# Kernel tuning notes

Hardware: AMD Instinct MI355X
Metric: run time of the kernel (lower is better)

Reference implementation:

```python
import jax, jax.numpy as jnp
import numpy as np

EPS = 1e-5
QMAX = 127.0


def fake_quant_int8(x):
    """Per-tensor symmetric int8 fake-quant (quantize+dequantize), dynamic scale.
    Mirrors brevitas Int8ActPerTensorFloat / Int8WeightPerTensorFloat math."""
    scale = jnp.maximum(jnp.max(jnp.abs(x)) / QMAX, 1e-8)
    q = jnp.clip(jnp.round(x / scale), -128.0, 127.0) * scale
    # straight-through estimator (identity grad through quant)
    return x + jax.lax.stop_gradient(q - x)


def layer_norm(x, g, b):
    mu = jnp.mean(x, axis=-1, keepdims=True)
    var = jnp.mean(jnp.square(x - mu), axis=-1, keepdims=True)
    return (x - mu) * jax.lax.rsqrt(var + EPS) * g + b


def setup_inputs() -> dict:
    key = jax.random.key(0)
    B, S, D, H = 64, 196, 768, 12
    M = 4 * D
    ks = jax.random.split(key, 8)
    s = lambda d: 1.0 / np.sqrt(d)
    return {
        "x": jax.random.normal(ks[0], (B, S, D), jnp.float32),
        "ln1_g": jnp.ones((D,), jnp.float32),
        "ln1_b": jnp.zeros((D,), jnp.float32),
        "ln2_g": jnp.ones((D,), jnp.float32),
        "ln2_b": jnp.zeros((D,), jnp.float32),
        "w_qkv": jax.random.normal(ks[1], (D, 3 * D), jnp.float32) * s(D),
        "b_qkv": jnp.zeros((3 * D,), jnp.float32),
        "w_o": jax.random.normal(ks[2], (D, D), jnp.float32) * s(D),
        "b_o": jnp.zeros((D,), jnp.float32),
        "w1": jax.random.normal(ks[3], (D, M), jnp.float32) * s(D),
        "b1": jnp.zeros((M,), jnp.float32),
        "w2": jax.random.normal(ks[4], (M, D), jnp.float32) * s(M),
        "b2": jnp.zeros((D,), jnp.float32),
    }


def _block(x, ln1_g, ln1_b, ln2_g, ln2_b, w_qkv, b_qkv, w_o, b_o, w1, b1, w2, b2):
    B, S, D = x.shape
    H = 12
    hd = D // H

    # --- LN -> quant -> MHSA -> add ---
    r1 = x
    h = fake_quant_int8(layer_norm(x, ln1_g, ln1_b))
    qkv = jnp.einsum("bsd,de->bse", h, fake_quant_int8(w_qkv)) + b_qkv
    q, k, v = jnp.split(qkv, 3, axis=-1)
    q = q.reshape(B, S, H, hd)
    k = k.reshape(B, S, H, hd)
    v = v.reshape(B, S, H, hd)
    logits = jnp.einsum("bqhd,bkhd->bhqk", q, k) / jnp.sqrt(jnp.float32(hd))
    attn = jax.nn.softmax(logits, axis=-1)
    ctx = jnp.einsum("bhqk,bkhd->bqhd", attn, v).reshape(B, S, D)
    ctx = fake_quant_int8(ctx)
    mhsa = jnp.einsum("bsd,de->bse", ctx, fake_quant_int8(w_o)) + b_o
    x = mhsa + r1

    # --- LN -> quant -> MLP (fc1 -> GELU -> quant -> fc2) -> add ---
    r2 = x
    h = fake_quant_int8(layer_norm(x, ln2_g, ln2_b))
    h = jnp.einsum("bsd,dm->bsm", h, fake_quant_int8(w1)) + b1
    h = jax.nn.gelu(h, approximate=False)  # torch nn.GELU default = exact erf
    h = fake_quant_int8(h)
    h = jnp.einsum("bsm,md->bsd", h, fake_quant_int8(w2)) + b2
    return h + r2


def reference(x, ln1_g, ln1_b, ln2_g, ln2_b, w_qkv, b_qkv, w_o, b_o, w1, b1, w2, b2):
    return _block(x, ln1_g, ln1_b, ln2_g, ln2_b, w_qkv, b_qkv, w_o, b_o, w1, b1, w2, b2)
```

## Files before the change

kernel.cpp:

```cpp
#include <hip/hip_runtime.h>
#include <cstdint>
#include <cstddef>

#define DEVFN __device__ __forceinline__

typedef short bf16x8 __attribute__((ext_vector_type(8)));
typedef float f32x4  __attribute__((ext_vector_type(4)));
typedef int   i32x4  __attribute__((ext_vector_type(4)));

static constexpr int NTOK  = 64 * 196;
static constexpr int DMODEL= 768;
static constexpr int NHEAD = 12;
static constexpr int NQKV  = 2304;
static constexpr int MMLP  = 3072;
static constexpr int SEQ   = 196;
static constexpr int NBATCH= 64;

enum { SL_LN1=0, SL_WQKV=1, SL_CTX=2, SL_WO=3, SL_LN2=4, SL_W1=5, SL_GELU=6, SL_W2=7 };

static constexpr int NSH       = 64;
static constexpr int SH_STRIDE = 64;
static constexpr int SLOTS_U32 = NSH * SH_STRIDE;

DEVFN float bf2f(unsigned short u){ return __uint_as_float(((unsigned)u) << 16); }
DEVFN unsigned short f2bf(float f){
  unsigned u = __float_as_uint(f);
  u += 0x7fffu + ((u >> 16) & 1u);
  return (unsigned short)(u >> 16);
}
DEVFN void split_bf(float v, unsigned short& hi, unsigned short& lo){
  hi = f2bf(v);
  lo = f2bf(v - bf2f(hi));
}
DEVFN float slot_absmax(const unsigned* __restrict__ slots, int slot){
  unsigned m = 0u;
#pragma unroll
  for (int j = 0; j < NSH; j++){
    unsigned u = slots[j * SH_STRIDE + slot];
    m = (u > m) ? u : m;
  }
  return __uint_as_float(m);
}
DEVFN float slot_scale(const unsigned* __restrict__ slots, int slot){
  return fmaxf(slot_absmax(slots, slot) / 127.0f, 1e-8f);
}
DEVFN void scatter_amax(unsigned* slots, int slot, unsigned bucket, float v){
  atomicMax(slots + (bucket & (NSH - 1)) * SH_STRIDE + slot, __float_as_uint(v));
}
DEVFN float quantval(float x, float s){
  float q = rintf(x / s);
  return fminf(fmaxf(q, -128.0f), 127.0f);
}
DEVFN unsigned pack4(float a, float b, float c, float d){
  return  ((unsigned)(unsigned char)(char)(int)a)
        | ((unsigned)(unsigned char)(char)(int)b << 8)
        | ((unsigned)(unsigned char)(char)(int)c << 16)
        | ((unsigned)(unsigned char)(char)(int)d << 24);
}
DEVFN float gelu_fast(float v){
  float s  = v * 0.70710678118654752f;
  float ax = fabsf(s);
  float t  = __builtin_amdgcn_rcpf(fmaf(0.3275911f, ax, 1.0f));
  float p  = t * fmaf(t, fmaf(t, fmaf(t, fmaf(t, 1.061405429f, -1.453152027f),
                                      1.421413741f), -0.284496736f), 0.254829592f);
  float er = fmaf(-p, __expf(-ax * ax), 1.0f);
  unsigned sgn = __float_as_uint(s) & 0x80000000u;
  er = __uint_as_float(__float_as_uint(er) | sgn);
  return 0.5f * v * (1.0f + er);
}
DEVFN f32x4 mfma16(bf16x8 a, bf16x8 b, f32x4 c){
  return __builtin_amdgcn_mfma_f32_16x16x32_bf16(a, b, c, 0, 0, 0);
}
DEVFN i32x4 mfma16i8(i32x4 a, i32x4 b, i32x4 c){
  return __builtin_amdgcn_mfma_i32_16x16x64_i8(a, b, c, 0, 0, 0);
}
DEVFN void async_ld16(const void* g, void* lds){
  __builtin_amdgcn_global_load_lds((const __attribute__((address_space(1))) void*)g,
                                   (__attribute__((address_space(3))) void*)lds, 16, 0, 0);
}
DEVFN int vidx(int d, int s){
  return d * 256 + (s ^ (((d ^ (d >> 2)) & 7) << 3));
}

__global__ void k_init(unsigned* slots){
  int i = blockIdx.x * blockDim.x + threadIdx.x;
  if (i < SLOTS_U32) slots[i] = 0u;
}

__global__ void k_absmax4(const float* __restrict__ x0, const float* __restrict__ x1,
                          const float* __restrict__ x2, const float* __restrict__ x3,
                          unsigned* slots){
  int bid = blockIdx.x;
  const float* x; int n4, slot, b0, nb;
  if (bid < 256)      { x = x0; n4 = DMODEL * NQKV  / 4; slot = SL_WQKV; b0 = 0;   nb = 256; }
  else if (bid < 384) { x = x1; n4 = DMODEL * DMODEL/ 4; slot = SL_WO;   b0 = 256; nb = 128; }
  else if (bid < 640) { x = x2; n4 = DMODEL * MMLP  / 4; slot = SL_W1;   b0 = 384; nb = 256; }
  else                { x = x3; n4 = MMLP   * DMODEL/ 4; slot = SL_W2;   b0 = 640; nb = 256; }
  int lb = bid - b0;
  float m = 0.f;
  const float4* x4 = (const float4*)x;
  int stride = nb * blockDim.x;
  for (int j = lb * blockDim.x + threadIdx.x; j < n4; j += stride){
    float4 v = x4[j];
    m = fmaxf(m, fmaxf(fmaxf(fabsf(v.x), fabsf(v.y)), fmaxf(fabsf(v.z), fabsf(v.w))));
  }
  for (int off = 32; off; off >>= 1) m = fmaxf(m, __shfl_xor(m, off));
  __shared__ float wm[4];
  int lane = threadIdx.x & 63, w = threadIdx.x >> 6;
  if (lane == 0) wm[w] = m;
  __syncthreads();
  if (threadIdx.x == 0){
    float bm = fmaxf(fmaxf(wm[0], wm[1]), fmaxf(wm[2], wm[3]));
    scatter_amax(slots, slot, bid, bm);
  }
}

__global__ void k_quant_transpose(const float* __restrict__ w, char* __restrict__ wt,
                                  int K, int N, const unsigned* __restrict__ slots, int slot){
  __shared__ float tile[32][33];
  float s = slot_scale(slots, slot);
  int n0 = blockIdx.x * 32, k0 = blockIdx.y * 32;
  int tx = threadIdx.x & 31, ty = threadIdx.x >> 5;
#pragma unroll
  for (int i = 0; i < 4; i++){
    int k = k0 + ty + i * 8;
    float v = w[(size_t)k * N + n0 + tx];
    tile[ty + i * 8][tx] = quantval(v, s);
  }
  __syncthreads();
  int n = threadIdx.x >> 3, kg = threadIdx.x & 7;
  unsigned o = pack4(tile[kg * 4 + 0][n], tile[kg * 4 + 1][n],
                     tile[kg * 4 + 2][n], tile[kg * 4 + 3][n]);
  *(unsigned*)(wt + (size_t)(n0 + n) * K + k0 + kg * 4) = o;
}

__global__ void k_layernorm(const float* __restrict__ x, const float* __restrict__ g,
                            const float* __restrict__ b, float* __restrict__ out,
                            unsigned* slots, int slot){
  int w = threadIdx.x >> 6, lane = threadIdx.x & 63;
  int row = blockIdx.x * 4 + w;
  const float4* xr = (const float4*)(x + (size_t)row * DMODEL);
  float4 v[3];
  float sum = 0.f;
#pragma unroll
  for (int i = 0; i < 3; i++){ v[i] = xr[i * 64 + lane]; sum += v[i].x + v[i].y + v[i].z + v[i].w; }
  for (int off = 32; off; off >>= 1) sum += __shfl_xor(sum, off);
  float mu = sum * (1.0f / 768.0f);
  float vs = 0.f;
#pragma unroll
  for (int i = 0; i < 3; i++){
    float dx = v[i].x - mu, dy = v[i].y - mu, dz = v[i].z - mu, dw = v[i].w - mu;
    vs += dx * dx + dy * dy + dz * dz + dw * dw;
  }
  for (int off = 32; off; off >>= 1) vs += __shfl_xor(vs, off);
  float inv = 1.0f / sqrtf(vs * (1.0f / 768.0f) + 1e-5f);
  const float4* g4 = (const float4*)g; const float4* b4 = (const float4*)b;
  float4* o4 = (float4*)(out + (size_t)row * DMODEL);
  float am = 0.f;
#pragma unroll
  for (int i = 0; i < 3; i++){
    float4 gg = g4[i * 64 + lane], bb = b4[i * 64 + lane], o;
    o.x = (v[i].x - mu) * inv * gg.x + bb.x;
    o.y = (v[i].y - mu) * inv * gg.y + bb.y;
    o.z = (v[i].z - mu) * inv * gg.z + bb.z;
    o.w = (v[i].w - mu) * inv * gg.w + bb.w;
    am = fmaxf(am, fmaxf(fmaxf(fabsf(o.x), fabsf(o.y)), fmaxf(fabsf(o.z), fabsf(o.w))));
    o4[i * 64 + lane] = o;
  }
  for (int off = 32; off; off >>= 1) am = fmaxf(am, __shfl_xor(am, off));
  __shared__ float am4[4];
  if (lane == 0) am4[w] = am;
  __syncthreads();
  if (threadIdx.x == 0){
    float bm = fmaxf(fmaxf(am4[0], am4[1]), fmaxf(am4[2], am4[3]));
    scatter_amax(slots, slot, blockIdx.x, bm);
  }
}

__global__ void k_quant_act(const float* __restrict__ x, unsigned* __restrict__ out,
                            int n4, const unsigned* __restrict__ slots, int slot){
  float s = slot_scale(slots, slot);
  const float4* x4 = (const float4*)x;
  int stride = gridDim.x * blockDim.x;
  for (int j = blockIdx.x * blockDim.x + threadIdx.x; j < n4; j += stride){
    float4 v = x4[j];
    out[j] = pack4(quantval(v.x, s), quantval(v.y, s), quantval(v.z, s), quantval(v.w, s));
  }
}

__global__ void k_quant_bf16_i8(const unsigned short* __restrict__ x, unsigned* __restrict__ out,
                                int n4, const unsigned* __restrict__ slots, int slot){
  float s = slot_scale(slots, slot);
  const ushort4* x4 = (const ushort4*)x;
  int stride = gridDim.x * blockDim.x;
  for (int j = blockIdx.x * blockDim.x + threadIdx.x; j < n4; j += stride){
    ushort4 v = x4[j];
    out[j] = pack4(quantval(bf2f(v.x), s), quantval(bf2f(v.y), s),
                   quantval(bf2f(v.z), s), quantval(bf2f(v.w), s));
  }
}

template<int EPI>
__launch_bounds__(256, 4)
__global__ void k_gemm(const char* __restrict__ A,
                       const char* __restrict__ Bt,
                       const float* __restrict__ bias,
                       const float* __restrict__ res,
                       float* __restrict__ Cf,
                       unsigned short* __restrict__ Cb,
                       const unsigned* __restrict__ slots, int sa_slot, int sb_slot,
                       unsigned* gmax_slots, int gmax_slot,
                       int M, int N, int K)
{
  __shared__ __align__(16) char smem[32768];
  __shared__ float gm4[4];
  const int tid  = threadIdx.x;
  const int lane = tid & 63;
  const int wv   = tid >> 6;
  const int wx   = wv & 1, wy = wv >> 1;
  const int quad = lane >> 4;
  const int l16  = lane & 15;
  const int m0 = blockIdx.y * 128, n0 = blockIdx.x * 128;

  auto issue = [&](int k0, int buf){
#pragma unroll
    for (int i = 0; i < 2; i++){
      int c = tid + i * 256;
      int row = c >> 2, q = c & 3;
      int qs = (q - ((row + (row >> 2)) & 3)) & 3;
      async_ld16(A + (size_t)(m0 + row) * K + k0 + qs * 16,
                 smem + buf * 8192 + (i * 256 + wv * 64) * 16);
    }
#pragma unroll
    for (int i = 0; i < 2; i++){
      int c = tid + i * 256;
      int row = c >> 2, q = c & 3;
      int qs = (q - ((row + (row >> 2)) & 3)) & 3;
      async_ld16(Bt + (size_t)(n0 + row) * K + k0 + qs * 16,
                 smem + 16384 + buf * 8192 + (i * 256 + wv * 64) * 16);
    }
  };

  i32x4 acc[4][4] = {};
  const int nk = K >> 6;
  issue(0, 0);

  const int ch = (((quad + (l16 & 3) + (l16 >> 2)) & 3)) * 16;

  for (int k = 0; k < nk; k++){
    const int cur = k & 1;
    if (k + 1 < nk){
      issue((k + 1) << 6, cur ^ 1);
      asm volatile("s_waitcnt vmcnt(4)" ::: "memory");
    } else {
      asm volatile("s_waitcnt vmcnt(0)" ::: "memory");
    }
    asm volatile("s_barrier" ::: "memory");

    const char* Ab = smem + cur * 8192;
    const char* Bb = smem + 16384 + cur * 8192;
    i32x4 af[4], bfr[4];
#pragma unroll
    for (int i = 0; i < 4; i++)
      af[i] = *(const i32x4*)(Ab + (wy * 64 + i * 16 + l16) * 64 + ch);
#pragma unroll
    for (int j = 0; j < 4; j++)
      bfr[j] = *(const i32x4*)(Bb + (wx * 64 + j * 16 + l16) * 64 + ch);
    asm volatile("s_waitcnt lgkmcnt(0)" ::: "memory");
    asm volatile("s_barrier" ::: "memory");

#pragma unroll
    for (int i = 0; i < 4; i++)
#pragma unroll
      for (int j = 0; j < 4; j++)
        acc[i][j] = mfma16i8(af[i], bfr[j], acc[i][j]);
  }
  __syncthreads();

  float (*stage)[132] = (float (*)[132])smem;
  const float sc = slot_scale(slots, sa_slot) * slot_scale(slots, sb_slot);
  const int col4 = (tid & 31) * 4;
  const int gc   = n0 + col4;
  const float4 bb = *(const float4*)&bias[gc];
  float gmax = 0.f;
#pragma unroll
  for (int i = 0; i < 4; i++){
#pragma unroll
    for (int j = 0; j < 4; j++)
#pragma unroll
      for (int r = 0; r < 4; r++)
        stage[wy * 16 + quad * 4 + r][wx * 64 + j * 16 + l16] = (float)acc[i][j][r];
    __syncthreads();
#pragma unroll
    for (int rr = 0; rr < 4; rr++){
      const int rl = rr * 8 + (tid >> 5);
      const int gm = m0 + ((rl >> 4) * 64) + i * 16 + (rl & 15);
      float4 v = *(const float4*)&stage[rl][col4];
      v.x = v.x * sc + bb.x; v.y = v.y * sc + bb.y;
      v.z = v.z * sc + bb.z; v.w = v.w * sc + bb.w;
      if constexpr (EPI == 1){
        float4 rv = *(const float4*)&res[(size_t)gm * N + gc];
        v.x += rv.x; v.y += rv.y; v.z += rv.z; v.w += rv.w;
        *(float4*)&Cf[(size_t)gm * N + gc] = v;
      } else if constexpr (EPI == 2){
        float g0 = gelu_fast(v.x);
        float g1 = gelu_fast(v.y);
        float g2 = gelu_fast(v.z);
        float g3 = gelu_fast(v.w);
        gmax = fmaxf(gmax, fmaxf(fmaxf(fabsf(g0), fabsf(g1)), fmaxf(fabsf(g2), fabsf(g3))));
        ushort4 o = {f2bf(g0), f2bf(g1), f2bf(g2), f2bf(g3)};
        *(ushort4*)&Cb[(size_t)gm * N + gc] = o;
      } else {
        *(float4*)&Cf[(size_t)gm * N + gc] = v;
      }
    }
    __syncthreads();
  }
  if constexpr (EPI == 2){
    for (int off = 32; off; off >>= 1) gmax = fmaxf(gmax, __shfl_xor(gmax, off));
    if (lane == 0) gm4[wv] = gmax;
    __syncthreads();
    if (tid == 0){
      float bm = fmaxf(fmaxf(gm4[0], gm4[1]), fmaxf(gm4[2], gm4[3]));
      scatter_amax(gmax_slots, gmax_slot, blockIdx.x + blockIdx.y * gridDim.x, bm);
    }
  }
}

__launch_bounds__(512, 2)
__global__ void k_attention(const float* __restrict__ qkv, float* __restrict__ ctx,
                            unsigned* slots){
  __shared__ __align__(16) unsigned short Khi[208 * 72], Klo[208 * 72];
  __shared__ __align__(16) unsigned short Vhi[64 * 256], Vlo[64 * 256];
  __shared__ __align__(16) unsigned short Ps[8][2][16 * 40];
  __shared__ float gm8[8];

  const int bh = blockIdx.x;
  const int b = bh / NHEAD, h = bh % NHEAD;
  const float* base = qkv + (size_t)b * SEQ * NQKV;
  const int tid = threadIdx.x, lane = tid & 63, wv = tid >> 6;
  const int quad = lane >> 4, l16 = lane & 15;

  float4 kreg[7], vreg[8];
#pragma unroll
  for (int i = 0; i < 7; i++){
    int idx = tid + i * 512;
    int r = idx >> 4, c4 = (idx & 15) * 4;
    float4 v = {0.f, 0.f, 0.f, 0.f};
    if (idx < 208 * 16 && r < SEQ)
      v = *(const float4*)(base + (size_t)r * NQKV + DMODEL + h * 64 + c4);
    kreg[i] = v;
  }
#pragma unroll
  for (int i = 0; i < 8; i++){
    int idx = tid + i * 512;
    int s = idx >> 4, dg = (idx & 15) * 4;
    float4 v = {0.f, 0.f, 0.f, 0.f};
    if (idx < 232 * 16 && s < SEQ)
      v = *(const float4*)(base + (size_t)s * NQKV + 2 * DMODEL + h * 64 + dg);
    vreg[i] = v;
  }
#pragma unroll
  for (int i = 0; i < 7; i++){
    int idx = tid + i * 512;
    if (idx < 208 * 16){
      int r = idx >> 4, c4 = (idx & 15) * 4;
      float4 v = kreg[i];
      unsigned short h0,l0,h1,l1,h2,l2,h3,l3;
      split_bf(v.x, h0, l0); split_bf(v.y, h1, l1); split_bf(v.z, h2, l2); split_bf(v.w, h3, l3);
      ushort4 hs = {h0, h1, h2, h3}, ls = {l0, l1, l2, l3};
      *(ushort4*)(Khi + r * 72 + c4) = hs;
      *(ushort4*)(Klo + r * 72 + c4) = ls;
    }
  }
#pragma unroll
  for (int i = 0; i < 8; i++){
    int idx = tid + i * 512;
    if (idx < 232 * 16){
      int s = idx >> 4, dg = (idx & 15) * 4;
      float4 v = vreg[i];
      unsigned short hi, lo;
      split_bf(v.x, hi, lo); Vhi[vidx(dg + 0, s)] = hi; Vlo[vidx(dg + 0, s)] = lo;
      split_bf(v.y, hi, lo); Vhi[vidx(dg + 1, s)] = hi; Vlo[vidx(dg + 1, s)] = lo;
      split_bf(v.z, hi, lo); Vhi[vidx(dg + 2, s)] = hi; Vlo[vidx(dg + 2, s)] = lo;
      split_bf(v.w, hi, lo); Vhi[vidx(dg + 3, s)] = hi; Vlo[vidx(dg + 3, s)] = lo;
    }
  }
  __syncthreads();

  unsigned short* PsH = &Ps[wv][0][0];
  unsigned short* PsL = &Ps[wv][1][0];

  float gmax = 0.f;
  for (int qt = wv; qt < 13; qt += 8){
    const int q0 = qt * 16;
    const int sq = q0 + l16;
    const bool valid = sq < SEQ;

    bf16x8 aqh[2], aql[2];
    const float* qrow = base + (size_t)(valid ? sq : 0) * NQKV + h * 64;
#pragma unroll
    for (int ks = 0; ks < 2; ks++){
      float4 v0 = {0,0,0,0}, v1 = {0,0,0,0};
      if (valid){
        v0 = *(const float4*)(qrow + ks * 32 + quad * 8);
        v1 = *(const float4*)(qrow + ks * 32 + quad * 8 + 4);
      }
      float vv[8] = {v0.x, v0.y, v0.z, v0.w, v1.x, v1.y, v1.z, v1.w};
#pragma unroll
      for (int j = 0; j < 8; j++){
        unsigned short hi, lo; split_bf(vv[j], hi, lo);
        aqh[ks][j] = (short)hi; aql[ks][j] = (short)lo;
      }
    }

    f32x4 sacc[13];
#pragma unroll
    for (int t = 0; t < 13; t++){
      f32x4 a = {0.f, 0.f, 0.f, 0.f};
#pragma unroll
      for (int ks = 0; ks < 2; ks++){
        bf16x8 bkh = *(const bf16x8*)(Khi + (t * 16 + l16) * 72 + ks * 32 + quad * 8);
        bf16x8 bkl = *(const bf16x8*)(Klo + (t * 16 + l16) * 72 + ks * 32 + quad * 8);
        a = mfma16(aqh[ks], bkh, a);
        a = mfma16(aqh[ks], bkl, a);
        a = mfma16(aql[ks], bkh, a);
      }
      sacc[t] = a;
    }

    float mx[4] = {-1e30f, -1e30f, -1e30f, -1e30f};
#pragma unroll
    for (int t = 0; t < 13; t++){
      bool dead = (t == 12) && (l16 >= 4);
#pragma unroll
      for (int r = 0; r < 4; r++){
        float v = dead ? -1e30f : sacc[t][r] * 0.125f;
        sacc[t][r] = v;
        mx[r] = fmaxf(mx[r], v);
      }
    }
#pragma unroll
    for (int off = 1; off < 16; off <<= 1)
#pragma unroll
      for (int r = 0; r < 4; r++) mx[r] = fmaxf(mx[r], __shfl_xor(mx[r], off));
    float sum[4] = {0.f, 0.f, 0.f, 0.f};
#pragma unroll
    for (int t = 0; t < 13; t++)
#pragma unroll
      for (int r = 0; r < 4; r++){
        float e = __expf(sacc[t][r] - mx[r]);
        sacc[t][r] = e; sum[r] += e;
      }
#pragma unroll
    for (int off = 1; off < 16; off <<= 1)
#pragma unroll
      for (int r = 0; r < 4; r++) sum[r] += __shfl_xor(sum[r], off);
    float inv[4];
#pragma unroll
    for (int r = 0; r < 4; r++) inv[r] = 1.0f / sum[r];

    f32x4 oacc[4] = {};
#pragma unroll
    for (int ks = 0; ks < 7; ks++){
      const int t0 = 2 * ks, t1 = 2 * ks + 1;
#pragma unroll
      for (int r = 0; r < 4; r++){
        int row = quad * 4 + r;
        unsigned short hi, lo;
        split_bf(sacc[t0][r] * inv[r], hi, lo);
        PsH[row * 40 + l16] = hi; PsL[row * 40 + l16] = lo;
        if (t1 < 13){
          split_bf(sacc[t1][r] * inv[r], hi, lo);
          PsH[row * 40 + 16 + l16] = hi; PsL[row * 40 + 16 + l16] = lo;
        } else {
          PsH[row * 40 + 16 + l16] = 0; PsL[row * 40 + 16 + l16] = 0;
        }
      }
      __builtin_amdgcn_wave_barrier();
      bf16x8 aph = *(const bf16x8*)(PsH + l16 * 40 + quad * 8);
      bf16x8 apl = *(const bf16x8*)(PsL + l16 * 40 + quad * 8);
#pragma unroll
      for (int n = 0; n < 4; n++){
        bf16x8 bvh = *(const bf16x8*)(Vhi + vidx(n * 16 + l16, ks * 32 + quad * 8));
        bf16x8 bvl = *(const bf16x8*)(Vlo + vidx(n * 16 + l16, ks * 32 + quad * 8));
        oacc[n] = mfma16(aph, bvh, oacc[n]);
        oacc[n] = mfma16(aph, bvl, oacc[n]);
        oacc[n] = mfma16(apl, bvh, oacc[n]);
      }
      __builtin_amdgcn_wave_barrier();
    }

#pragma unroll
    for (int r = 0; r < 4; r++){
      int srow = q0 + quad * 4 + r;
      if (srow < SEQ){
#pragma unroll
        for (int n = 0; n < 4; n++){
          float v = oacc[n][r];
          ctx[((size_t)(b * SEQ + srow)) * DMODEL + h * 64 + n * 16 + l16] = v;
          gmax = fmaxf(gmax, fabsf(v));
        }
      }
    }
  }
  for (int off = 32; off; off >>= 1) gmax = fmaxf(gmax, __shfl_xor(gmax, off));
  if (lane == 0) gm8[wv] = gmax;
  __syncthreads();
  if (tid == 0){
    float bm = 0.f;
#pragma unroll
    for (int i = 0; i < 8; i++) bm = fmaxf(bm, gm8[i]);
    scatter_amax(slots, SL_CTX, blockIdx.x, bm);
  }
}

extern "C" void kernel_launch(void* const* d_in, const int* in_sizes, int n_in,
                              void* d_out, int out_size, void* d_ws, size_t ws_size,
                              hipStream_t stream)
{
  const float* x     = (const float*)d_in[0];
  const float* ln1_g = (const float*)d_in[1];
  const float* ln1_b = (const float*)d_in[2];
  const float* ln2_g = (const float*)d_in[3];
  const float* ln2_b = (const float*)d_in[4];
  const float* w_qkv = (const float*)d_in[5];
  const float* b_qkv = (const float*)d_in[6];
  const float* w_o   = (const float*)d_in[7];
  const float* b_o   = (const float*)d_in[8];
  const float* w1    = (const float*)d_in[9];
  const float* b1    = (const float*)d_in[10];
  const float* w2    = (const float*)d_in[11];
  const float* b2    = (const float*)d_in[12];

  char* ws = (char*)d_ws;
  size_t off = 0;
  unsigned* slots = (unsigned*)ws;                 off += SLOTS_U32 * 4;
  char* wqkvT = (char*)(ws + off); off += (size_t)NQKV  * DMODEL;
  char* woT   = (char*)(ws + off); off += (size_t)DMODEL* DMODEL;
  char* w1T   = (char*)(ws + off); off += (size_t)MMLP  * DMODEL;
  char* w2T   = (char*)(ws + off); off += (size_t)DMODEL* MMLP;
  off = (off + 255) & ~(size_t)255;
  float* t1    = (float*)(ws + off);               off += (size_t)NTOK * DMODEL * 4;
  char*  t1q   = (char*)(ws + off);                off += (size_t)NTOK * DMODEL;
  off = (off + 255) & ~(size_t)255;
  float* qkv   = (float*)(ws + off);               off += (size_t)NTOK * NQKV * 4;
  float* xmid  = (float*)(ws + off);               off += (size_t)NTOK * DMODEL * 4;
  unsigned short* h1 = (unsigned short*)qkv;
  char* h1q = (char*)qkv + (size_t)NTOK * MMLP * 2;
  float* outp = (float*)d_out;

  k_init<<<(SLOTS_U32 + 255) / 256, 256, 0, stream>>>(slots);

  k_absmax4<<<896, 256, 0, stream>>>(w_qkv, w_o, w1, w2, slots);

  k_quant_transpose<<<dim3(NQKV / 32, DMODEL / 32), 256, 0, stream>>>(w_qkv, wqkvT, DMODEL, NQKV, slots, SL_WQKV);
  k_quant_transpose<<<dim3(DMODEL / 32, DMODEL / 32), 256, 0, stream>>>(w_o, woT, DMODEL, DMODEL, slots, SL_WO);
  k_quant_transpose<<<dim3(MMLP / 32, DMODEL / 32), 256, 0, stream>>>(w1, w1T, DMODEL, MMLP, slots, SL_W1);
  k_quant_transpose<<<dim3(DMODEL / 32, MMLP / 32), 256, 0, stream>>>(w2, w2T, MMLP, DMODEL, slots, SL_W2);

  k_layernorm<<<NTOK / 4, 256, 0, stream>>>(x, ln1_g, ln1_b, t1, slots, SL_LN1);
  {
    int n4 = NTOK * DMODEL / 4;
    k_quant_act<<<(n4 + 255) / 256, 256, 0, stream>>>(t1, (unsigned*)t1q, n4, slots, SL_LN1);
  }
  k_gemm<0><<<dim3(NQKV / 128, NTOK / 128), 256, 0, stream>>>(
      t1q, wqkvT, b_qkv, nullptr, qkv, nullptr, slots, SL_LN1, SL_WQKV, nullptr, 0,
      NTOK, NQKV, DMODEL);

  k_attention<<<NBATCH * NHEAD, 512, 0, stream>>>(qkv, t1, slots);
  {
    int n4 = NTOK * DMODEL / 4;
    k_quant_act<<<(n4 + 255) / 256, 256, 0, stream>>>(t1, (unsigned*)t1q, n4, slots, SL_CTX);
  }
  k_gemm<1><<<dim3(DMODEL / 128, NTOK / 128), 256, 0, stream>>>(
      t1q, woT, b_o, x, xmid, nullptr, slots, SL_CTX, SL_WO, nullptr, 0,
      NTOK, DMODEL, DMODEL);

  k_layernorm<<<NTOK / 4, 256, 0, stream>>>(xmid, ln2_g, ln2_b, t1, slots, SL_LN2);
  {
    int n4 = NTOK * DMODEL / 4;
    k_quant_act<<<(n4 + 255) / 256, 256, 0, stream>>>(t1, (unsigned*)t1q, n4, slots, SL_LN2);
  }
  k_gemm<2><<<dim3(MMLP / 128, NTOK / 128), 256, 0, stream>>>(
      t1q, w1T, b1, nullptr, nullptr, h1, slots, SL_LN2, SL_W1, slots, SL_GELU,
      NTOK, MMLP, DMODEL);
  {
    int n4 = NTOK * MMLP / 4;
    k_quant_bf16_i8<<<(n4 + 255) / 256, 256, 0, stream>>>(h1, (unsigned*)h1q, n4, slots, SL_GELU);
  }
  k_gemm<1><<<dim3(DMODEL / 128, NTOK / 128), 256, 0, stream>>>(
      h1q, w2T, b2, xmid, outp, nullptr, slots, SL_GELU, SL_W2, nullptr, 0,
      NTOK, DMODEL, MMLP);
}
```

Baseline: 500.9 us.

## Use one wave per query tile in attention, merge weight quant launches, cap quant grids

Attention now launches 13 waves per block so each wave handles exactly one 16-row query tile, removing the two-round imbalance of 8 waves over 13 tiles. MFMA loops are bracketed with s_setprio to favour matrix issue. The four weight quantize-transpose launches are merged into one kernel, and the elementwise quant kernels use a fixed 2048-block grid. Larger blocks raise register pressure under the new launch bounds, and the fixed grid relies on the quant kernels striding over the whole tensor.

```diff
diff --git a/kernel.cpp b/kernel.cpp
--- a/kernel.cpp
+++ b/kernel.cpp
@@ -115,11 +115,23 @@
   }
 }
 
-__global__ void k_quant_transpose(const float* __restrict__ w, char* __restrict__ wt,
-                                  int K, int N, const unsigned* __restrict__ slots, int slot){
+__global__ void k_quant_transpose4(const float* __restrict__ w0, const float* __restrict__ w1,
+                                   const float* __restrict__ w2, const float* __restrict__ w3,
+                                   char* __restrict__ t0, char* __restrict__ t1,
+                                   char* __restrict__ t2, char* __restrict__ t3,
+                                   const unsigned* __restrict__ slots){
+  int bid = blockIdx.x;
+  const float* w; char* wt; int K, N, slot, lb;
+  if (bid < 1728)      { w = w0; wt = t0; K = DMODEL; N = NQKV;   slot = SL_WQKV; lb = bid; }
+  else if (bid < 2304) { w = w1; wt = t1; K = DMODEL; N = DMODEL; slot = SL_WO;   lb = bid - 1728; }
+  else if (bid < 4608) { w = w2; wt = t2; K = DMODEL; N = MMLP;   slot = SL_W1;   lb = bid - 2304; }
+  else                 { w = w3; wt = t3; K = MMLP;   N = DMODEL; slot = SL_W2;   lb = bid - 4608; }
+  int nx = N / 32;
+  int bx = lb % nx, by = lb / nx;
+
   __shared__ float tile[32][33];
   float s = slot_scale(slots, slot);
-  int n0 = blockIdx.x * 32, k0 = blockIdx.y * 32;
+  int n0 = bx * 32, k0 = by * 32;
   int tx = threadIdx.x & 31, ty = threadIdx.x >> 5;
 #pragma unroll
   for (int i = 0; i < 4; i++){
@@ -327,13 +339,13 @@
   }
 }
 
-__launch_bounds__(512, 2)
+__launch_bounds__(832, 4)
 __global__ void k_attention(const float* __restrict__ qkv, float* __restrict__ ctx,
                             unsigned* slots){
   __shared__ __align__(16) unsigned short Khi[208 * 72], Klo[208 * 72];
   __shared__ __align__(16) unsigned short Vhi[64 * 256], Vlo[64 * 256];
-  __shared__ __align__(16) unsigned short Ps[8][2][16 * 40];
-  __shared__ float gm8[8];
+  __shared__ __align__(16) unsigned short Ps[13][2][16 * 40];
+  __shared__ float gm[13];
 
   const int bh = blockIdx.x;
   const int b = bh / NHEAD, h = bh % NHEAD;
@@ -341,19 +353,18 @@
   const int tid = threadIdx.x, lane = tid & 63, wv = tid >> 6;
   const int quad = lane >> 4, l16 = lane & 15;
 
-  float4 kreg[7], vreg[8];
-#pragma unroll
-  for (int i = 0; i < 7; i++){
-    int idx = tid + i * 512;
+  float4 kreg[4], vreg[5];
+#pragma unroll
+  for (int i = 0; i < 4; i++){
+    int idx = tid + i * 832;
     int r = idx >> 4, c4 = (idx & 15) * 4;
     float4 v = {0.f, 0.f, 0.f, 0.f};
-    if (idx < 208 * 16 && r < SEQ)
-      v = *(const float4*)(base + (size_t)r * NQKV + DMODEL + h * 64 + c4);
+    if (r < SEQ) v = *(const float4*)(base + (size_t)r * NQKV + DMODEL + h * 64 + c4);
     kreg[i] = v;
   }
 #pragma unroll
-  for (int i = 0; i < 8; i++){
-    int idx = tid + i * 512;
+  for (int i = 0; i < 5; i++){
+    int idx = tid + i * 832;
     int s = idx >> 4, dg = (idx & 15) * 4;
     float4 v = {0.f, 0.f, 0.f, 0.f};
     if (idx < 232 * 16 && s < SEQ)
@@ -361,21 +372,19 @@
     vreg[i] = v;
   }
 #pragma unroll
-  for (int i = 0; i < 7; i++){
-    int idx = tid + i * 512;
-    if (idx < 208 * 16){
-      int r = idx >> 4, c4 = (idx & 15) * 4;
-      float4 v = kreg[i];
-      unsigned short h0,l0,h1,l1,h2,l2,h3,l3;
-      split_bf(v.x, h0, l0); split_bf(v.y, h1, l1); split_bf(v.z, h2, l2); split_bf(v.w, h3, l3);
-      ushort4 hs = {h0, h1, h2, h3}, ls = {l0, l1, l2, l3};
-      *(ushort4*)(Khi + r * 72 + c4) = hs;
-      *(ushort4*)(Klo + r * 72 + c4) = ls;
-    }
-  }
-#pragma unroll
-  for (int i = 0; i < 8; i++){
-    int idx = tid + i * 512;
+  for (int i = 0; i < 4; i++){
+    int idx = tid + i * 832;
+    int r = idx >> 4, c4 = (idx & 15) * 4;
+    float4 v = kreg[i];
+    unsigned short h0,l0,h1,l1,h2,l2,h3,l3;
+    split_bf(v.x, h0, l0); split_bf(v.y, h1, l1); split_bf(v.z, h2, l2); split_bf(v.w, h3, l3);
+    ushort4 hs = {h0, h1, h2, h3}, ls = {l0, l1, l2, l3};
+    *(ushort4*)(Khi + r * 72 + c4) = hs;
+    *(ushort4*)(Klo + r * 72 + c4) = ls;
+  }
+#pragma unroll
+  for (int i = 0; i < 5; i++){
+    int idx = tid + i * 832;
     if (idx < 232 * 16){
       int s = idx >> 4, dg = (idx & 15) * 4;
       float4 v = vreg[i];
@@ -392,7 +401,8 @@
   unsigned short* PsL = &Ps[wv][1][0];
 
   float gmax = 0.f;
-  for (int qt = wv; qt < 13; qt += 8){
+  const int qt = wv;
+  {
     const int q0 = qt * 16;
     const int sq = q0 + l16;
     const bool valid = sq < SEQ;
@@ -415,6 +425,7 @@
     }
 
     f32x4 sacc[13];
+    __builtin_amdgcn_s_setprio(1);
 #pragma unroll
     for (int t = 0; t < 13; t++){
       f32x4 a = {0.f, 0.f, 0.f, 0.f};
@@ -428,6 +439,7 @@
       }
       sacc[t] = a;
     }
+    __builtin_amdgcn_s_setprio(0);
 
     float mx[4] = {-1e30f, -1e30f, -1e30f, -1e30f};
 #pragma unroll
@@ -480,6 +492,7 @@
       __builtin_amdgcn_wave_barrier();
       bf16x8 aph = *(const bf16x8*)(PsH + l16 * 40 + quad * 8);
       bf16x8 apl = *(const bf16x8*)(PsL + l16 * 40 + quad * 8);
+      __builtin_amdgcn_s_setprio(1);
 #pragma unroll
       for (int n = 0; n < 4; n++){
         bf16x8 bvh = *(const bf16x8*)(Vhi + vidx(n * 16 + l16, ks * 32 + quad * 8));
@@ -488,6 +501,7 @@
         oacc[n] = mfma16(aph, bvl, oacc[n]);
         oacc[n] = mfma16(apl, bvh, oacc[n]);
       }
+      __builtin_amdgcn_s_setprio(0);
       __builtin_amdgcn_wave_barrier();
     }
 
@@ -505,12 +519,12 @@
     }
   }
   for (int off = 32; off; off >>= 1) gmax = fmaxf(gmax, __shfl_xor(gmax, off));
-  if (lane == 0) gm8[wv] = gmax;
+  if (lane == 0) gm[wv] = gmax;
   __syncthreads();
   if (tid == 0){
     float bm = 0.f;
 #pragma unroll
-    for (int i = 0; i < 8; i++) bm = fmaxf(bm, gm8[i]);
+    for (int i = 0; i < 13; i++) bm = fmaxf(bm, gm[i]);
     scatter_amax(slots, SL_CTX, blockIdx.x, bm);
   }
 }
@@ -554,24 +568,22 @@
 
   k_absmax4<<<896, 256, 0, stream>>>(w_qkv, w_o, w1, w2, slots);
 
-  k_quant_transpose<<<dim3(NQKV / 32, DMODEL / 32), 256, 0, stream>>>(w_qkv, wqkvT, DMODEL, NQKV, slots, SL_WQKV);
-  k_quant_transpose<<<dim3(DMODEL / 32, DMODEL / 32), 256, 0, stream>>>(w_o, woT, DMODEL, DMODEL, slots, SL_WO);
-  k_quant_transpose<<<dim3(MMLP / 32, DMODEL / 32), 256, 0, stream>>>(w1, w1T, DMODEL, MMLP, slots, SL_W1);
-  k_quant_transpose<<<dim3(DMODEL / 32, MMLP / 32), 256, 0, stream>>>(w2, w2T, MMLP, DMODEL, slots, SL_W2);
+  k_quant_transpose4<<<6912, 256, 0, stream>>>(w_qkv, w_o, w1, w2,
+                                               wqkvT, woT, w1T, w2T, slots);
 
   k_layernorm<<<NTOK / 4, 256, 0, stream>>>(x, ln1_g, ln1_b, t1, slots, SL_LN1);
   {
     int n4 = NTOK * DMODEL / 4;
-    k_quant_act<<<(n4 + 255) / 256, 256, 0, stream>>>(t1, (unsigned*)t1q, n4, slots, SL_LN1);
+    k_quant_act<<<2048, 256, 0, stream>>>(t1, (unsigned*)t1q, n4, slots, SL_LN1);
   }
   k_gemm<0><<<dim3(NQKV / 128, NTOK / 128), 256, 0, stream>>>(
       t1q, wqkvT, b_qkv, nullptr, qkv, nullptr, slots, SL_LN1, SL_WQKV, nullptr, 0,
       NTOK, NQKV, DMODEL);
 
-  k_attention<<<NBATCH * NHEAD, 512, 0, stream>>>(qkv, t1, slots);
+  k_attention<<<NBATCH * NHEAD, 832, 0, stream>>>(qkv, t1, slots);
   {
     int n4 = NTOK * DMODEL / 4;
-    k_quant_act<<<(n4 + 255) / 256, 256, 0, stream>>>(t1, (unsigned*)t1q, n4, slots, SL_CTX);
+    k_quant_act<<<2048, 256, 0, stream>>>(t1, (unsigned*)t1q, n4, slots, SL_CTX);
   }
   k_gemm<1><<<dim3(DMODEL / 128, NTOK / 128), 256, 0, stream>>>(
       t1q, woT, b_o, x, xmid, nullptr, slots, SL_CTX, SL_WO, nullptr, 0,
@@ -580,14 +592,14 @@
   k_layernorm<<<NTOK / 4, 256, 0, stream>>>(xmid, ln2_g, ln2_b, t1, slots, SL_LN2);
   {
     int n4 = NTOK * DMODEL / 4;
-    k_quant_act<<<(n4 + 255) / 256, 256, 0, stream>>>(t1, (unsigned*)t1q, n4, slots, SL_LN2);
+    k_quant_act<<<2048, 256, 0, stream>>>(t1, (unsigned*)t1q, n4, slots, SL_LN2);
   }
   k_gemm<2><<<dim3(MMLP / 128, NTOK / 128), 256, 0, stream>>>(
       t1q, w1T, b1, nullptr, nullptr, h1, slots, SL_LN2, SL_W1, slots, SL_GELU,
       NTOK, MMLP, DMODEL);
   {
     int n4 = NTOK * MMLP / 4;
-    k_quant_bf16_i8<<<(n4 + 255) / 256, 256, 0, stream>>>(h1, (unsigned*)h1q, n4, slots, SL_GELU);
+    k_quant_bf16_i8<<<2048, 256, 0, stream>>>(h1, (unsigned*)h1q, n4, slots, SL_GELU);
   }
   k_gemm<1><<<dim3(DMODEL / 128, NTOK / 128), 256, 0, stream>>>(
       h1q, w2T, b2, xmid, outp, nullptr, slots, SL_GELU, SL_W2, nullptr, 0,
```

Result: faster. 468.0 us (-6.6%).
